# Performance work log

Hardware: AMD Instinct MI355X
Metric: run time of the kernel (lower is better)

The kernel has to match this reference:

```python
import jax, jax.numpy as jnp
import numpy as np

B, N, NPOINT, K = 8, 4096, 512, 32
D_IN, D_POS, D_OUT = 64, 64, 128
D = D_IN + D_POS  # 128, channel dim entering Double_SA
EPS = 1e-5


def _gather(pts, idx):
    # pts [B,N,C], idx [B,...] -> [B,...,C]
    return jax.vmap(lambda p, i: p[i])(pts, idx)


def _bn(x, p):
    # eval-mode BatchNorm over last (channel) dim; p = [gamma, beta, mean, var]
    g, b, m, v = p
    return g * (x - m) * jax.lax.rsqrt(v + EPS) + b


def _fps(xyz, start):
    # iterative farthest point sampling, vectorized over batch
    Bb, Nn, _ = xyz.shape
    def step(carry, _):
        dist, far = carry  # dist [B,N], far [B]
        c = jnp.take_along_axis(xyz, far[:, None, None], axis=1)  # [B,1,3]
        d = jnp.sum((xyz - c) ** 2, -1)
        dist = jnp.minimum(dist, d)
        return (dist, jnp.argmax(dist, -1)), far
    init = (jnp.full((Bb, Nn), 1e10, xyz.dtype), start)
    _, idx = jax.lax.scan(step, init, None, length=NPOINT)
    return idx.T  # [B, NPOINT]


def _forward(xyz, points, fps_start, pos_w1, pos_b1, pos_bn1, pos_w2, pos_b2, pos_bn2,
             nsa_wq, nsa_bq, nsa_wk, nsa_bk, nsa_wv, nsa_bv, nsa_gamma, gam_gamma,
             cat_w1, cat_b1, cat_bn1, cat_w2, cat_b2, cat_bn2, sc_w, sc_b, sc_bn):
    fps_idx = _fps(xyz, fps_start)                 # [B,S]
    center_xyz = _gather(xyz, fps_idx)             # [B,S,3]
    # brute-force KNN: squared distances center -> all points, take k smallest
    d2 = (jnp.sum(center_xyz ** 2, -1)[:, :, None] + jnp.sum(xyz ** 2, -1)[:, None, :]
          - 2.0 * jnp.einsum('bsc,bnc->bsn', center_xyz, xyz))  # [B,S,N]
    neg_d, knn_idx = jax.lax.top_k(-d2, K)
    knn_dist = -neg_d                               # [B,S,K], ascending
    grouped_xyz = _gather(xyz, knn_idx)             # [B,S,K,3]
    grouped_pts = _gather(points, knn_idx)          # [B,S,K,D_IN]
    # PosEmbeding: cat(center, neighbor, relative, dist) -> MLP(10 -> Dpos/2 -> Dpos)
    center = jnp.broadcast_to(center_xyz[:, :, None, :], grouped_xyz.shape)
    feat = jnp.concatenate([center, grouped_xyz, grouped_xyz - center, knn_dist[..., None]], -1)
    h = jax.nn.relu(_bn(feat @ pos_w1 + pos_b1, pos_bn1))
    pos = jax.nn.relu(_bn(h @ pos_w2 + pos_b2, pos_bn2))
    x = jnp.concatenate([pos, grouped_pts], -1)     # [B,S,K,D]
    # Neighbor_SA_New: per-group self-attention over K neighbors
    q = x @ nsa_wq + nsa_bq                         # [B,S,K,D//8]
    k = x @ nsa_wk + nsa_bk
    v = x @ nsa_wv + nsa_bv                         # [B,S,K,D]
    attn = jax.nn.softmax(jnp.einsum('bskc,bsjc->bskj', q, k), axis=-1)
    nei = nsa_gamma * jnp.einsum('bskj,bsjd->bskd', attn, v) + x
    # GAM: attention between groups over flattened K*D features
    flat = x.reshape(B, NPOINT, K * D)
    ga = jax.nn.softmax(jnp.einsum('bsd,btd->bst', flat, flat), axis=-1)  # [B,S,S]
    grp = gam_gamma * jnp.einsum('bst,btd->bsd', ga, flat).reshape(B, NPOINT, K, D) + x
    dsa = jnp.concatenate([nei, grp], -1)           # [B,S,K,2D]
    main = _bn(jax.nn.relu(_bn(dsa @ cat_w1 + cat_b1, cat_bn1)) @ cat_w2 + cat_b2, cat_bn2)
    sc = jax.nn.relu(_bn(grouped_pts @ sc_w + sc_b, sc_bn))
    new_points = jnp.max(jax.nn.relu(main + sc), axis=2)  # [B,S,D_OUT]
    return center_xyz, new_points


def setup_inputs():
    ks = jax.random.split(jax.random.key(0), 40)
    def w(i, shape, s=0.05):
        return s * jax.random.normal(ks[i], shape, jnp.float32)
    def bnp(i, c):
        k1, k2, k3, k4 = jax.random.split(ks[i], 4)
        return jnp.stack([jax.random.uniform(k1, (c,), jnp.float32, 0.5, 1.5),
                          0.1 * jax.random.normal(k2, (c,), jnp.float32),
                          0.1 * jax.random.normal(k3, (c,), jnp.float32),
                          jax.random.uniform(k4, (c,), jnp.float32, 0.5, 1.5)])
    return dict(
        xyz=jax.random.normal(ks[0], (B, N, 3), jnp.float32),
        points=jax.random.normal(ks[1], (B, N, D_IN), jnp.float32),
        fps_start=jax.random.randint(ks[2], (B,), 0, N),
        pos_w1=w(3, (10, D_POS // 2)), pos_b1=w(4, (D_POS // 2,)), pos_bn1=bnp(5, D_POS // 2),
        pos_w2=w(6, (D_POS // 2, D_POS)), pos_b2=w(7, (D_POS,)), pos_bn2=bnp(8, D_POS),
        nsa_wq=w(9, (D, D // 8)), nsa_bq=w(10, (D // 8,)),
        nsa_wk=w(11, (D, D // 8)), nsa_bk=w(12, (D // 8,)),
        nsa_wv=w(13, (D, D)), nsa_bv=w(14, (D,)),
        nsa_gamma=jnp.array([0.5], jnp.float32),
        gam_gamma=jnp.array([0.5], jnp.float32),
        cat_w1=w(15, (2 * D, 2 * D)), cat_b1=w(16, (2 * D,)), cat_bn1=bnp(17, 2 * D),
        cat_w2=w(18, (2 * D, D_OUT)), cat_b2=w(19, (D_OUT,)), cat_bn2=bnp(20, D_OUT),
        sc_w=w(21, (D_IN, D_OUT)), sc_b=w(22, (D_OUT,)), sc_bn=bnp(23, D_OUT),
    )


def reference(xyz, points, fps_start, pos_w1, pos_b1, pos_bn1, pos_w2, pos_b2, pos_bn2,
              nsa_wq, nsa_bq, nsa_wk, nsa_bk, nsa_wv, nsa_bv, nsa_gamma, gam_gamma,
              cat_w1, cat_b1, cat_bn1, cat_w2, cat_b2, cat_bn2, sc_w, sc_b, sc_bn):
    return _forward(xyz, points, fps_start, pos_w1, pos_b1, pos_bn1, pos_w2, pos_b2, pos_bn2,
                    nsa_wq, nsa_bq, nsa_wk, nsa_bk, nsa_wv, nsa_bv, nsa_gamma, gam_gamma,
                    cat_w1, cat_b1, cat_bn1, cat_w2, cat_b2, cat_bn2, sc_w, sc_b, sc_bn)
```

## Files before the change

### kernel.cpp

```cpp
#include <hip/hip_runtime.h>
#include <stdint.h>
#include <float.h>

typedef unsigned int uint;

#define NB 8
#define NPTS 4096
#define NS 512
#define NKN 32

__device__ int   g_fps_idx[NB*NS];
__device__ int   g_knn_idx[NB*NS*NKN];
__device__ float g_knn_d2 [NB*NS*NKN];
__device__ float g_posb   [(size_t)NB*NS*NKN*64];
__device__ float g_ga     [(size_t)NB*NS*NS];
__device__ float g_dsa    [(size_t)NB*NS*NKN*256];

__device__ __forceinline__ unsigned long long shfl_down_u64(unsigned long long v, int off){
  int lo = __shfl_down((int)(unsigned)v, off);
  int hi = __shfl_down((int)(unsigned)(v >> 32), off);
  return ((unsigned long long)(unsigned)hi << 32) | (unsigned)lo;
}
__device__ __forceinline__ unsigned long long u64max(unsigned long long a, unsigned long long b){
  return a > b ? a : b;
}
__device__ __forceinline__ unsigned long long u64min(unsigned long long a, unsigned long long b){
  return a < b ? a : b;
}
__device__ __forceinline__ void ldf8(const float* p, float* d){
  float4 a = *(const float4*)p, b = *(const float4*)(p+4);
  d[0]=a.x; d[1]=a.y; d[2]=a.z; d[3]=a.w; d[4]=b.x; d[5]=b.y; d[6]=b.z; d[7]=b.w;
}
__device__ __forceinline__ int read_start(const int* __restrict__ start, int b){
  int w1 = start[1], w3 = start[3], w5 = start[5], w7 = start[7];
  bool is64 = ((w1 | w3 | w5 | w7) == 0);
  int v = is64 ? start[2*b] : start[b];
  return v & (NPTS - 1);
}

__device__ __forceinline__ void load_flat8(const float* __restrict__ points,
                                           int b, int row, int n, float* d){
  const int k = n >> 7, col = n & 63;
  if (n & 64){
    const int idx = g_knn_idx[((b << 9) + row)*32 + k];
    ldf8(points + (((size_t)b << 12) + idx)*64 + col, d);
  } else {
    ldf8(g_posb + (((size_t)((b << 9) + row))*32 + k)*64 + col, d);
  }
}
__device__ __forceinline__ float4 load_flat4(const float* __restrict__ points,
                                             int b, int row, int n){
  const int k = n >> 7, d = n & 127;
  if (d & 64){
    const int idx = g_knn_idx[((b << 9) + row)*32 + k];
    return *(const float4*)(points + (((size_t)b << 12) + idx)*64 + (d & 63));
  } else {
    return *(const float4*)(g_posb + (((size_t)((b << 9) + row))*32 + k)*64 + d);
  }
}
__device__ __forceinline__ void load_gram8(const float* __restrict__ points,
                                           int b, int row, int kc, float* d){
  if (kc < 2048){
    ldf8(g_posb + ((size_t)((b << 9) + row))*2048 + kc, d);
  } else {
    const int kc2 = kc - 2048, kg = kc2 >> 6, col = kc2 & 63;
    const int idx = g_knn_idx[((b << 9) + row)*32 + kg];
    ldf8(points + (((size_t)b << 12) + idx)*64 + col, d);
  }
}

__global__ __launch_bounds__(256) void k_fps(const float* __restrict__ xyz,
                                             const int* __restrict__ start,
                                             float* __restrict__ center_out){
#pragma clang fp contract(off)
  const int b = blockIdx.x, tid = threadIdx.x;
  const float* X = xyz + (size_t)b * NPTS * 3;
  __shared__ float sx[NPTS], sy[NPTS], sz[NPTS];
  for (int p = tid; p < NPTS; p += 256){
    sx[p] = X[3*p]; sy[p] = X[3*p+1]; sz[p] = X[3*p+2];
  }
  __shared__ int s_start0;
  if (tid == 0) s_start0 = read_start(start, b);
  __syncthreads();
  float px[16], py[16], pz[16], dist[16];
  for (int i = 0; i < 16; i++){
    int p = tid*16 + i;
    px[i] = sx[p]; py[i] = sy[p]; pz[i] = sz[p];
    dist[i] = 1e10f;
  }
  __shared__ unsigned long long s_k[2][4];
  int cur = s_start0;
  for (int t = 0; t < NS; t++){
    if (tid == 0){
      g_fps_idx[b*NS + t] = cur;
      center_out[(size_t)(b*NS + t)*3 + 0] = sx[cur];
      center_out[(size_t)(b*NS + t)*3 + 1] = sy[cur];
      center_out[(size_t)(b*NS + t)*3 + 2] = sz[cur];
    }
    const float cx = sx[cur], cy = sy[cur], cz = sz[cur];
    unsigned long long k_[16];
#pragma unroll
    for (int i = 0; i < 16; i++){
      float dx = px[i]-cx, dy = py[i]-cy, dz = pz[i]-cz;
      float d = ((dx*dx) + (dy*dy)) + (dz*dz);
      dist[i] = fminf(dist[i], d);
      k_[i] = ((unsigned long long)__float_as_uint(dist[i]) << 32)
            | (unsigned)(NPTS-1 - (tid*16 + i));
    }
#pragma unroll
    for (int st = 8; st; st >>= 1)
      for (int i = 0; i < st; i++) k_[i] = u64max(k_[i], k_[i+st]);
    unsigned long long bk = k_[0];
    { unsigned long long a = shfl_down_u64(bk,16), c = shfl_down_u64(bk,32), d = shfl_down_u64(bk,48);
      bk = u64max(u64max(bk,a), u64max(c,d)); }
    { unsigned long long a = shfl_down_u64(bk,4),  c = shfl_down_u64(bk,8),  d = shfl_down_u64(bk,12);
      bk = u64max(u64max(bk,a), u64max(c,d)); }
    { unsigned long long a = shfl_down_u64(bk,1),  c = shfl_down_u64(bk,2),  d = shfl_down_u64(bk,3);
      bk = u64max(u64max(bk,a), u64max(c,d)); }
    const int par = t & 1;
    if ((tid & 63) == 0) s_k[par][tid>>6] = bk;
    __syncthreads();
    unsigned long long m = u64max(u64max(s_k[par][0], s_k[par][1]),
                                  u64max(s_k[par][2], s_k[par][3]));
    cur = NPTS-1 - (int)(unsigned)m;
  }
}

__global__ __launch_bounds__(256) void k_knn(const float* __restrict__ xyz){
#pragma clang fp contract(off)
  const int g = blockIdx.x;
  const int b = g >> 9;
  const int tid = threadIdx.x;
  const float* X = xyz + (size_t)b * NPTS * 3;
  const int cidx = g_fps_idx[g];
  const float cx = X[3*cidx], cy = X[3*cidx+1], cz = X[3*cidx+2];
  const float cs = ((cx*cx) + (cy*cy)) + (cz*cz);
  unsigned long long kl[16];
#pragma unroll
  for (int i = 0; i < 16; i++){
    int p = tid*16 + i;
    float x = X[3*p], y = X[3*p+1], z = X[3*p+2];
    float xs2 = ((x*x) + (y*y)) + (z*z);
    float dt  = ((cx*x) + (cy*y)) + (cz*z);
    float d   = (cs + xs2) - 2.0f*dt;
    unsigned bits = __float_as_uint(d);
    unsigned mono = (bits & 0x80000000u) ? ~bits : (bits ^ 0x80000000u);
    kl[i] = ((unsigned long long)mono << 32) | (unsigned)p;
  }
  __shared__ unsigned long long s_w[2][4];
  unsigned long long last = 0;
  for (int sel = 0; sel < NKN; sel++){
    unsigned long long mk[16];
#pragma unroll
    for (int i = 0; i < 16; i++)
      mk[i] = (kl[i] > last) ? kl[i] : 0xFFFFFFFFFFFFFFFFULL;
#pragma unroll
    for (int st = 8; st; st >>= 1)
      for (int i = 0; i < st; i++) mk[i] = u64min(mk[i], mk[i+st]);
    unsigned long long bk = mk[0];
    { unsigned long long a = shfl_down_u64(bk,16), c = shfl_down_u64(bk,32), d = shfl_down_u64(bk,48);
      bk = u64min(u64min(bk,a), u64min(c,d)); }
    { unsigned long long a = shfl_down_u64(bk,4),  c = shfl_down_u64(bk,8),  d = shfl_down_u64(bk,12);
      bk = u64min(u64min(bk,a), u64min(c,d)); }
    { unsigned long long a = shfl_down_u64(bk,1),  c = shfl_down_u64(bk,2),  d = shfl_down_u64(bk,3);
      bk = u64min(u64min(bk,a), u64min(c,d)); }
    const int par = sel & 1;
    if ((tid & 63) == 0) s_w[par][tid>>6] = bk;
    __syncthreads();
    unsigned long long m = u64min(u64min(s_w[par][0], s_w[par][1]),
                                  u64min(s_w[par][2], s_w[par][3]));
    last = m;
    if (tid == 0){
      unsigned hm = (unsigned)(m >> 32);
      unsigned bits = (hm & 0x80000000u) ? (hm ^ 0x80000000u) : ~hm;
      g_knn_idx[g*NKN + sel] = (int)(unsigned)m;
      g_knn_d2 [g*NKN + sel] = __uint_as_float(bits);
    }
  }
}

__global__ __launch_bounds__(256) void k_posembed(
    const float* __restrict__ xyz,
    const float* __restrict__ w1, const float* __restrict__ b1, const float* __restrict__ bn1,
    const float* __restrict__ w2, const float* __restrict__ b2, const float* __restrict__ bn2){
  __shared__ float w1s[320], a1s[32], d1s[32], w2s[2048], a2s[64], d2s[64];
  const int t = threadIdx.x;
  for (int i = t; i < 320; i += 256) w1s[i] = w1[i];
  for (int i = t; i < 2048; i += 256) w2s[i] = w2[i];
  if (t < 32){
    float g = bn1[t], be = bn1[32+t], m = bn1[64+t], v = bn1[96+t];
    float a = g * rsqrtf(v + 1e-5f);
    a1s[t] = a; d1s[t] = b1[t]*a + (be - m*a);
  }
  if (t < 64){
    float g = bn2[t], be = bn2[64+t], m = bn2[128+t], v = bn2[192+t];
    float a = g * rsqrtf(v + 1e-5f);
    a2s[t] = a; d2s[t] = b2[t]*a + (be - m*a);
  }
  __syncthreads();
  const int row = blockIdx.x*256 + t;
  const int b = row >> 14;
  const int g = row >> 5;
  const float* X = xyz + (size_t)b * NPTS * 3;
  const int ci = g_fps_idx[g];
  const int ni = g_knn_idx[row];
  float c0 = X[3*ci], c1 = X[3*ci+1], c2 = X[3*ci+2];
  float n0 = X[3*ni], n1 = X[3*ni+1], n2 = X[3*ni+2];
  float feat[10] = {c0,c1,c2, n0,n1,n2, n0-c0,n1-c1,n2-c2, g_knn_d2[row]};
  float h[32];
  for (int o = 0; o < 32; o++){
    float acc = 0.f;
    for (int j = 0; j < 10; j++) acc += feat[j]*w1s[j*32+o];
    h[o] = fmaxf(acc*a1s[o] + d1s[o], 0.f);
  }
  float* xr = g_posb + (size_t)row * 64;
  for (int o = 0; o < 64; o++){
    float acc = 0.f;
    for (int j = 0; j < 32; j++) acc += h[j]*w2s[j*64+o];
    xr[o] = fmaxf(acc*a2s[o] + d2s[o], 0.f);
  }
}

__global__ __launch_bounds__(256) void k_gram(const float* __restrict__ points){
  const int b = blockIdx.y;
  int ti = 0, rem = blockIdx.x;
  while (rem >= 8 - ti){ rem -= 8 - ti; ti++; }
  const int tj = ti + rem;
  const int i0 = ti * 64, j0 = tj * 64;
  __shared__ float As[32][68];
  __shared__ float Bs[32][68];
  const int t = threadIdx.x, tx = t & 15, ty = t >> 4;
  float acc[4][4] = {};
  for (int k0 = 0; k0 < 4096; k0 += 32){
    {
      int r = t >> 2, kk = (t & 3) * 8;
      float ta[8], tb[8];
      load_gram8(points, b, i0+r, k0+kk, ta);
      load_gram8(points, b, j0+r, k0+kk, tb);
      for (int jj = 0; jj < 8; jj++){
        int k = kk + jj;
        int c = (r + (k & 24)) & 63;
        As[k][c] = ta[jj]; Bs[k][c] = tb[jj];
      }
    }
    __syncthreads();
    for (int kk = 0; kk < 32; kk++){
      const int rot = kk & 24;
      const float4 a4 = *(const float4*)(&As[kk][(ty*4 + rot) & 63]);
      const float4 b4 = *(const float4*)(&Bs[kk][(tx*4 + rot) & 63]);
      const float ar[4] = {a4.x,a4.y,a4.z,a4.w};
      const float br[4] = {b4.x,b4.y,b4.z,b4.w};
      for (int ia = 0; ia < 4; ia++)
        for (int ib = 0; ib < 4; ib++) acc[ia][ib] += ar[ia]*br[ib];
    }
    __syncthreads();
  }
  float* C = g_ga + (size_t)b * NS * NS;
  for (int ia = 0; ia < 4; ia++){
    float4 o = {acc[ia][0], acc[ia][1], acc[ia][2], acc[ia][3]};
    *(float4*)(C + (size_t)(i0+ty*4+ia)*NS + j0 + tx*4) = o;
  }
  if (ti != tj){
    for (int ib = 0; ib < 4; ib++){
      float4 o = {acc[0][ib], acc[1][ib], acc[2][ib], acc[3][ib]};
      *(float4*)(C + (size_t)(j0+tx*4+ib)*NS + i0 + ty*4) = o;
    }
  }
}

__global__ __launch_bounds__(256) void k_softmax(){
  float* R = g_ga + (size_t)blockIdx.x * NS;
  const int t = threadIdx.x;
  float v0 = R[t], v1 = R[t+256];
  __shared__ float sm[4], ssum[4];
  float m = fmaxf(v0, v1);
  for (int off = 32; off; off >>= 1) m = fmaxf(m, __shfl_down(m, off));
  if ((t & 63) == 0) sm[t>>6] = m;
  __syncthreads();
  float mm = fmaxf(fmaxf(sm[0], sm[1]), fmaxf(sm[2], sm[3]));
  float e0 = expf(v0 - mm), e1 = expf(v1 - mm);
  float s = e0 + e1;
  for (int off = 32; off; off >>= 1) s += __shfl_down(s, off);
  if ((t & 63) == 0) ssum[t>>6] = s;
  __syncthreads();
  float inv = 1.0f / (ssum[0]+ssum[1]+ssum[2]+ssum[3]);
  R[t] = e0*inv; R[t+256] = e1*inv;
}

__global__ __launch_bounds__(256) void k_grp(const float* __restrict__ points,
                                             const float* __restrict__ gam_g){
  const int b = blockIdx.y;
  const int s0 = (blockIdx.x >> 6) * 64, n0 = (blockIdx.x & 63) * 64;
  const float* G = g_ga + (size_t)b * NS * NS;
  __shared__ float As[32][68];
  __shared__ float Bs[32][68];
  const int t = threadIdx.x, tx = t & 15, ty = t >> 4;
  float acc[4][4] = {};
  for (int k0 = 0; k0 < NS; k0 += 32){
    {
      int r = t >> 2, kk = (t & 3) * 8;
      const float* pa = G + (size_t)(s0+r)*NS + k0 + kk;
      float4 v0 = *(const float4*)pa, v1 = *(const float4*)(pa+4);
      const float va[8] = {v0.x,v0.y,v0.z,v0.w,v1.x,v1.y,v1.z,v1.w};
      for (int jj = 0; jj < 8; jj++){
        int k = kk + jj;
        As[k][(r + (k & 24)) & 63] = va[jj];
      }
      int k2 = t >> 3, c = (t & 7) * 8;
      float tb[8];
      load_flat8(points, b, k0+k2, n0+c, tb);
      float4 w0 = {tb[0],tb[1],tb[2],tb[3]}, w1 = {tb[4],tb[5],tb[6],tb[7]};
      *(float4*)(&Bs[k2][c])   = w0;
      *(float4*)(&Bs[k2][c+4]) = w1;
    }
    __syncthreads();
    for (int kk = 0; kk < 32; kk++){
      const float4 a4 = *(const float4*)(&As[kk][(ty*4 + (kk & 24)) & 63]);
      const float4 b4 = *(const float4*)(&Bs[kk][tx*4]);
      const float ar[4] = {a4.x,a4.y,a4.z,a4.w};
      const float br[4] = {b4.x,b4.y,b4.z,b4.w};
      for (int ia = 0; ia < 4; ia++)
        for (int ib = 0; ib < 4; ib++) acc[ia][ib] += ar[ia]*br[ib];
    }
    __syncthreads();
  }
  const float gmg = gam_g[0];
  const int n = n0 + tx*4;
  const int kq = n >> 7, dq = n & 127;
  for (int ia = 0; ia < 4; ia++){
    int s = s0 + ty*4 + ia;
    float4 xv = load_flat4(points, b, s, n);
    float4 o = {gmg*acc[ia][0]+xv.x, gmg*acc[ia][1]+xv.y,
                gmg*acc[ia][2]+xv.z, gmg*acc[ia][3]+xv.w};
    *(float4*)(g_dsa + ((size_t)((b*NS + s)*32 + kq))*256 + 128 + dq) = o;
  }
}

__global__ __launch_bounds__(256) void k_nsa(const float* __restrict__ points,
    const float* __restrict__ wq, const float* __restrict__ bq,
    const float* __restrict__ wk, const float* __restrict__ bk,
    const float* __restrict__ wv, const float* __restrict__ bv_,
    const float* __restrict__ nsa_g){
  const int g = blockIdx.y*512 + blockIdx.x;
  const int t = threadIdx.x, b = g >> 9;
  const int r = t >> 3, c = t & 7;
  __shared__ float xs[32][132];
  __shared__ float vs[32][132];
  __shared__ float qs[32][17], ks[32][17];
  __shared__ float at[32][33];
  {
    float tmp[8];
    ldf8(g_posb + ((size_t)g*32 + r)*64 + c*8, tmp);
    for (int j = 0; j < 8; j++) xs[r][c*8+j] = tmp[j];
    int idx = g_knn_idx[g*32 + r];
    ldf8(points + ((size_t)b*NPTS + idx)*64 + c*8, tmp);
    for (int j = 0; j < 8; j++) xs[r][64+c*8+j] = tmp[j];
  }
  __syncthreads();
  {
    float aq0 = bq[c], aq1 = bq[c+8], ak0 = bk[c], ak1 = bk[c+8];
    for (int j = 0; j < 128; j++){
      float xv = xs[r][j];
      aq0 += xv * wq[j*16+c];
      aq1 += xv * wq[j*16+c+8];
      ak0 += xv * wk[j*16+c];
      ak1 += xv * wk[j*16+c+8];
    }
    qs[r][c] = aq0; qs[r][c+8] = aq1; ks[r][c] = ak0; ks[r][c+8] = ak1;
  }
  {
    const float4* bv4 = (const float4*)bv_;
    float4 va = bv4[c], vb = bv4[8+c], vc = bv4[16+c], vd = bv4[24+c];
    const float4* wv4 = (const float4*)wv;
    for (int j = 0; j < 128; j++){
      float xv = xs[r][j];
      const float4* row = wv4 + (size_t)j*32;
      float4 w0 = row[c], w1 = row[8+c], w2 = row[16+c], w3 = row[24+c];
      va.x += xv*w0.x; va.y += xv*w0.y; va.z += xv*w0.z; va.w += xv*w0.w;
      vb.x += xv*w1.x; vb.y += xv*w1.y; vb.z += xv*w1.z; vb.w += xv*w1.w;
      vc.x += xv*w2.x; vc.y += xv*w2.y; vc.z += xv*w2.z; vc.w += xv*w2.w;
      vd.x += xv*w3.x; vd.y += xv*w3.y; vd.z += xv*w3.z; vd.w += xv*w3.w;
    }
    float4* vrow = (float4*)(&vs[r][0]);
    vrow[c] = va; vrow[8+c] = vb; vrow[16+c] = vc; vrow[24+c] = vd;
  }
  __syncthreads();
  float p0, p1, p2, p3;
  {
    float s[4];
    for (int jj = 0; jj < 4; jj++){
      int j = 4*c + jj; float acc = 0.f;
      for (int cc = 0; cc < 16; cc++) acc += qs[r][cc] * ks[j][cc];
      s[jj] = acc;
    }
    float m = fmaxf(fmaxf(s[0], s[1]), fmaxf(s[2], s[3]));
    m = fmaxf(m, __shfl_xor(m, 1));
    m = fmaxf(m, __shfl_xor(m, 2));
    m = fmaxf(m, __shfl_xor(m, 4));
    float e0 = expf(s[0]-m), e1 = expf(s[1]-m), e2 = expf(s[2]-m), e3 = expf(s[3]-m);
    float sum = ((e0 + e1) + (e2 + e3));
    sum += __shfl_xor(sum, 1);
    sum += __shfl_xor(sum, 2);
    sum += __shfl_xor(sum, 4);
    float inv = 1.0f / sum;
    p0 = e0*inv; p1 = e1*inv; p2 = e2*inv; p3 = e3*inv;
    at[r][4*c+0] = p0; at[r][4*c+1] = p1; at[r][4*c+2] = p2; at[r][4*c+3] = p3;
  }
  {
    float4 a0 = {0,0,0,0}, a1 = {0,0,0,0}, a2 = {0,0,0,0}, a3 = {0,0,0,0};
    for (int j = 0; j < 32; j++){
      float a = at[r][j];
      const float4* vrow = (const float4*)(&vs[j][0]);
      float4 w0 = vrow[c], w1 = vrow[8+c], w2 = vrow[16+c], w3 = vrow[24+c];
      a0.x += a*w0.x; a0.y += a*w0.y; a0.z += a*w0.z; a0.w += a*w0.w;
      a1.x += a*w1.x; a1.y += a*w1.y; a1.z += a*w1.z; a1.w += a*w1.w;
      a2.x += a*w2.x; a2.y += a*w2.y; a2.z += a*w2.z; a2.w += a*w2.w;
      a3.x += a*w3.x; a3.y += a*w3.y; a3.z += a*w3.z; a3.w += a*w3.w;
    }
    const float gmn = nsa_g[0];
    float* dst = g_dsa + ((size_t)g*32 + r)*256;
    float4 x0 = *(const float4*)(&xs[r][ 0+4*c]);
    float4 x1 = *(const float4*)(&xs[r][32+4*c]);
    float4 x2 = *(const float4*)(&xs[r][64+4*c]);
    float4 x3 = *(const float4*)(&xs[r][96+4*c]);
    float4 o0 = {gmn*a0.x+x0.x, gmn*a0.y+x0.y, gmn*a0.z+x0.z, gmn*a0.w+x0.w};
    float4 o1 = {gmn*a1.x+x1.x, gmn*a1.y+x1.y, gmn*a1.z+x1.z, gmn*a1.w+x1.w};
    float4 o2 = {gmn*a2.x+x2.x, gmn*a2.y+x2.y, gmn*a2.z+x2.z, gmn*a2.w+x2.w};
    float4 o3 = {gmn*a3.x+x3.x, gmn*a3.y+x3.y, gmn*a3.z+x3.z, gmn*a3.w+x3.w};
    *(float4*)(dst +  0 + 4*c) = o0;
    *(float4*)(dst + 32 + 4*c) = o1;
    *(float4*)(dst + 64 + 4*c) = o2;
    *(float4*)(dst + 96 + 4*c) = o3;
  }
}

__global__ __launch_bounds__(512) void k_mlp(const float* __restrict__ points,
    const float* __restrict__ w1, const float* __restrict__ b1, const float* __restrict__ bn1,
    const float* __restrict__ w2, const float* __restrict__ b2, const float* __restrict__ bn2,
    const float* __restrict__ wsc, const float* __restrict__ bsc, const float* __restrict__ bnsc,
    float* __restrict__ out){
  const int g = blockIdx.y*512 + blockIdx.x;
  const int t = threadIdx.x, b = g >> 9;
  __shared__ float ds[32][260];
  __shared__ float ps[32][68];
  __shared__ float a1s[256], d1s[256];
  __shared__ float red[512];
  for (int i = t; i < 2048; i += 512){
    int r = i >> 6, c = (i & 63) * 4;
    *(float4*)(&ds[r][c]) = *(const float4*)(g_dsa + ((size_t)g*32 + r)*256 + c);
  }
  if (t < 512){
    int r = t >> 4, c = (t & 15) * 4;
    int idx = g_knn_idx[g*32 + r];
    *(float4*)(&ps[r][c]) = *(const float4*)(points + ((size_t)b*NPTS + idx)*64 + c);
  }
  if (t < 256){
    float gg2 = bn1[t], be = bn1[256+t], m = bn1[512+t], v = bn1[768+t];
    float a = gg2 * rsqrtf(v + 1e-5f);
    a1s[t] = a; d1s[t] = b1[t]*a + (be - m*a);
  }
  __syncthreads();
  {
    const int kg = t >> 6, c0 = (t & 63) * 4;
    float acc[4][4] = {};
    for (int j = 0; j < 256; j += 4){
      float wvv[4][4];
      for (int jj = 0; jj < 4; jj++){
        float4 wrow = *(const float4*)(w1 + (j+jj)*256 + c0);
        wvv[jj][0] = wrow.x; wvv[jj][1] = wrow.y; wvv[jj][2] = wrow.z; wvv[jj][3] = wrow.w;
      }
      for (int r = 0; r < 4; r++){
        const float4 d4 = *(const float4*)(&ds[kg*4+r][j]);
        const float dr[4] = {d4.x, d4.y, d4.z, d4.w};
        for (int jj = 0; jj < 4; jj++)
          for (int i = 0; i < 4; i++) acc[r][i] += dr[jj]*wvv[jj][i];
      }
    }
    float4 o[4];
    for (int r = 0; r < 4; r++){
      o[r].x = fmaxf(acc[r][0]*a1s[c0+0] + d1s[c0+0], 0.f);
      o[r].y = fmaxf(acc[r][1]*a1s[c0+1] + d1s[c0+1], 0.f);
      o[r].z = fmaxf(acc[r][2]*a1s[c0+2] + d1s[c0+2], 0.f);
      o[r].w = fmaxf(acc[r][3]*a1s[c0+3] + d1s[c0+3], 0.f);
    }
    __syncthreads();
    for (int r = 0; r < 4; r++)
      *(float4*)(&ds[kg*4+r][c0]) = o[r];
  }
  __syncthreads();
  {
    const int c = t & 127, kh = t >> 7;
    float g2 = bn2[c], be2 = bn2[128+c], m2 = bn2[256+c], v2 = bn2[384+c];
    float a2 = g2 * rsqrtf(v2 + 1e-5f);
    float d2v = b2[c]*a2 + (be2 - m2*a2);
    float gsc = bnsc[c], besc = bnsc[128+c], msc = bnsc[256+c], vsc = bnsc[384+c];
    float asc = gsc * rsqrtf(vsc + 1e-5f);
    float dscv = bsc[c]*asc + (besc - msc*asc);
    float accm[8] = {};
    for (int j = 0; j < 256; j += 4){
      float w0 = w2[j*128+c], w1v = w2[(j+1)*128+c];
      float w2v = w2[(j+2)*128+c], w3 = w2[(j+3)*128+c];
      for (int r = 0; r < 8; r++){
        const float4 h4 = *(const float4*)(&ds[kh*8+r][j]);
        accm[r] += h4.x*w0; accm[r] += h4.y*w1v; accm[r] += h4.z*w2v; accm[r] += h4.w*w3;
      }
    }
    float accs[8] = {};
    for (int j = 0; j < 64; j += 4){
      float w0 = wsc[j*128+c], w1v = wsc[(j+1)*128+c];
      float w2v = wsc[(j+2)*128+c], w3 = wsc[(j+3)*128+c];
      for (int r = 0; r < 8; r++){
        const float4 p4 = *(const float4*)(&ps[kh*8+r][j]);
        accs[r] += p4.x*w0; accs[r] += p4.y*w1v; accs[r] += p4.z*w2v; accs[r] += p4.w*w3;
      }
    }
    float mx = -1e30f;
    for (int r = 0; r < 8; r++){
      float mainv = accm[r]*a2 + d2v;
      float scv = fmaxf(accs[r]*asc + dscv, 0.f);
      mx = fmaxf(mx, fmaxf(mainv + scv, 0.f));
    }
    red[t] = mx;
  }
  __syncthreads();
  if (t < 128){
    float m = fmaxf(fmaxf(red[t], red[t+128]), fmaxf(red[t+256], red[t+384]));
    out[12288 + (size_t)g*128 + t] = m;
  }
}

extern "C" void kernel_launch(void* const* d_in, const int* in_sizes, int n_in,
                              void* d_out, int out_size, void* d_ws, size_t ws_size,
                              hipStream_t stream){
  (void)in_sizes; (void)n_in; (void)d_ws; (void)ws_size; (void)out_size;
  const float* xyz      = (const float*)d_in[0];
  const float* points   = (const float*)d_in[1];
  const int*   fstart   = (const int*)  d_in[2];
  const float* pos_w1   = (const float*)d_in[3];
  const float* pos_b1   = (const float*)d_in[4];
  const float* pos_bn1  = (const float*)d_in[5];
  const float* pos_w2   = (const float*)d_in[6];
  const float* pos_b2   = (const float*)d_in[7];
  const float* pos_bn2  = (const float*)d_in[8];
  const float* nsa_wq   = (const float*)d_in[9];
  const float* nsa_bq   = (const float*)d_in[10];
  const float* nsa_wk   = (const float*)d_in[11];
  const float* nsa_bk   = (const float*)d_in[12];
  const float* nsa_wv   = (const float*)d_in[13];
  const float* nsa_bv   = (const float*)d_in[14];
  const float* nsa_g    = (const float*)d_in[15];
  const float* gam_g    = (const float*)d_in[16];
  const float* cat_w1   = (const float*)d_in[17];
  const float* cat_b1   = (const float*)d_in[18];
  const float* cat_bn1  = (const float*)d_in[19];
  const float* cat_w2   = (const float*)d_in[20];
  const float* cat_b2   = (const float*)d_in[21];
  const float* cat_bn2  = (const float*)d_in[22];
  const float* sc_w     = (const float*)d_in[23];
  const float* sc_b     = (const float*)d_in[24];
  const float* sc_bn    = (const float*)d_in[25];
  float* out = (float*)d_out;

  k_fps     <<<NB, 256, 0, stream>>>(xyz, fstart, out);
  k_knn     <<<NB*NS, 256, 0, stream>>>(xyz);
  k_posembed<<<512, 256, 0, stream>>>(xyz, pos_w1, pos_b1, pos_bn1, pos_w2, pos_b2, pos_bn2);
  k_gram    <<<dim3(36, NB), 256, 0, stream>>>(points);
  k_softmax <<<NB*NS, 256, 0, stream>>>();
  k_grp     <<<dim3(512, NB), 256, 0, stream>>>(points, gam_g);
  k_nsa     <<<dim3(512, NB), 256, 0, stream>>>(points, nsa_wq, nsa_bq, nsa_wk, nsa_bk,
                                                nsa_wv, nsa_bv, nsa_g);
  k_mlp     <<<dim3(512, NB), 512, 0, stream>>>(points, cat_w1, cat_b1, cat_bn1,
                                                cat_w2, cat_b2, cat_bn2,
                                                sc_w, sc_b, sc_bn, out);
}
```

Before: 1.967 ms.

## Enlarge k_grp register tile and retile k_mlp second GEMM for vector weight loads

k_grp now computes a 64x128 output tile per block with an 8x4 per-thread accumulator, up from a 64x64 tile with 4x4. This halves the grid and raises arithmetic intensity per shared-memory read. In k_mlp's second stage, each thread now computes 2 rows by 4 columns using float4 weight loads instead of scalar per-column loads across 8 rows, followed by a 16-way max reduction in shared memory. The larger tiles need more registers and shared memory, which may lower occupancy.

Result: slower. 2.072 ms (+5.3%).

```diff
diff --git a/kernel.cpp b/kernel.cpp
--- a/kernel.cpp
+++ b/kernel.cpp
@@ -290,12 +290,12 @@
 __global__ __launch_bounds__(256) void k_grp(const float* __restrict__ points,
                                              const float* __restrict__ gam_g){
   const int b = blockIdx.y;
-  const int s0 = (blockIdx.x >> 6) * 64, n0 = (blockIdx.x & 63) * 64;
+  const int s0 = (blockIdx.x >> 5) * 64, n0 = (blockIdx.x & 31) * 128;
   const float* G = g_ga + (size_t)b * NS * NS;
   __shared__ float As[32][68];
-  __shared__ float Bs[32][68];
-  const int t = threadIdx.x, tx = t & 15, ty = t >> 4;
-  float acc[4][4] = {};
+  __shared__ float Bs[32][132];
+  const int t = threadIdx.x, tx = t & 31, ry = t >> 5;
+  float acc[8][4] = {};
   for (int k0 = 0; k0 < NS; k0 += 32){
     {
       int r = t >> 2, kk = (t & 3) * 8;
@@ -306,20 +306,27 @@
         int k = kk + jj;
         As[k][(r + (k & 24)) & 63] = va[jj];
       }
-      int k2 = t >> 3, c = (t & 7) * 8;
-      float tb[8];
-      load_flat8(points, b, k0+k2, n0+c, tb);
-      float4 w0 = {tb[0],tb[1],tb[2],tb[3]}, w1 = {tb[4],tb[5],tb[6],tb[7]};
-      *(float4*)(&Bs[k2][c])   = w0;
-      *(float4*)(&Bs[k2][c+4]) = w1;
+      int k2 = t >> 3, c16 = (t & 7) * 16;
+      float tb[16];
+      load_flat8(points, b, k0+k2, n0+c16,     tb);
+      load_flat8(points, b, k0+k2, n0+c16+8, tb+8);
+      float4 w0 = {tb[0],tb[1],tb[2],tb[3]},   w1 = {tb[4],tb[5],tb[6],tb[7]};
+      float4 w2 = {tb[8],tb[9],tb[10],tb[11]}, w3 = {tb[12],tb[13],tb[14],tb[15]};
+      *(float4*)(&Bs[k2][c16])    = w0;
+      *(float4*)(&Bs[k2][c16+4])  = w1;
+      *(float4*)(&Bs[k2][c16+8])  = w2;
+      *(float4*)(&Bs[k2][c16+12]) = w3;
     }
     __syncthreads();
     for (int kk = 0; kk < 32; kk++){
-      const float4 a4 = *(const float4*)(&As[kk][(ty*4 + (kk & 24)) & 63]);
+      const int rot = kk & 24;
+      const int ca = (ry*8 + rot) & 63;
+      const float4 a0 = *(const float4*)(&As[kk][ca]);
+      const float4 a1 = *(const float4*)(&As[kk][ca+4]);
       const float4 b4 = *(const float4*)(&Bs[kk][tx*4]);
-      const float ar[4] = {a4.x,a4.y,a4.z,a4.w};
+      const float ar[8] = {a0.x,a0.y,a0.z,a0.w,a1.x,a1.y,a1.z,a1.w};
       const float br[4] = {b4.x,b4.y,b4.z,b4.w};
-      for (int ia = 0; ia < 4; ia++)
+      for (int ia = 0; ia < 8; ia++)
         for (int ib = 0; ib < 4; ib++) acc[ia][ib] += ar[ia]*br[ib];
     }
     __syncthreads();
@@ -327,8 +334,8 @@
   const float gmg = gam_g[0];
   const int n = n0 + tx*4;
   const int kq = n >> 7, dq = n & 127;
-  for (int ia = 0; ia < 4; ia++){
-    int s = s0 + ty*4 + ia;
+  for (int ia = 0; ia < 8; ia++){
+    int s = s0 + ry*8 + ia;
     float4 xv = load_flat4(points, b, s, n);
     float4 o = {gmg*acc[ia][0]+xv.x, gmg*acc[ia][1]+xv.y,
                 gmg*acc[ia][2]+xv.z, gmg*acc[ia][3]+xv.w};
@@ -444,12 +451,12 @@
   __shared__ float ds[32][260];
   __shared__ float ps[32][68];
   __shared__ float a1s[256], d1s[256];
-  __shared__ float red[512];
+  __shared__ float sm2[16][132];
   for (int i = t; i < 2048; i += 512){
     int r = i >> 6, c = (i & 63) * 4;
     *(float4*)(&ds[r][c]) = *(const float4*)(g_dsa + ((size_t)g*32 + r)*256 + c);
   }
-  if (t < 512){
+  {
     int r = t >> 4, c = (t & 15) * 4;
     int idx = g_knn_idx[g*32 + r];
     *(float4*)(&ps[r][c]) = *(const float4*)(points + ((size_t)b*NPTS + idx)*64 + c);
@@ -489,42 +496,66 @@
   }
   __syncthreads();
   {
-    const int c = t & 127, kh = t >> 7;
-    float g2 = bn2[c], be2 = bn2[128+c], m2 = bn2[256+c], v2 = bn2[384+c];
-    float a2 = g2 * rsqrtf(v2 + 1e-5f);
-    float d2v = b2[c]*a2 + (be2 - m2*a2);
-    float gsc = bnsc[c], besc = bnsc[128+c], msc = bnsc[256+c], vsc = bnsc[384+c];
-    float asc = gsc * rsqrtf(vsc + 1e-5f);
-    float dscv = bsc[c]*asc + (besc - msc*asc);
-    float accm[8] = {};
+    const int c0 = (t & 31) * 4, rg = t >> 5;
+    float accm0[4] = {}, accm1[4] = {};
     for (int j = 0; j < 256; j += 4){
-      float w0 = w2[j*128+c], w1v = w2[(j+1)*128+c];
-      float w2v = w2[(j+2)*128+c], w3 = w2[(j+3)*128+c];
-      for (int r = 0; r < 8; r++){
-        const float4 h4 = *(const float4*)(&ds[kh*8+r][j]);
-        accm[r] += h4.x*w0; accm[r] += h4.y*w1v; accm[r] += h4.z*w2v; accm[r] += h4.w*w3;
+      float4 wr0 = *(const float4*)(w2 + (size_t)(j+0)*128 + c0);
+      float4 wr1 = *(const float4*)(w2 + (size_t)(j+1)*128 + c0);
+      float4 wr2 = *(const float4*)(w2 + (size_t)(j+2)*128 + c0);
+      float4 wr3 = *(const float4*)(w2 + (size_t)(j+3)*128 + c0);
+      const float wA[4] = {wr0.x, wr0.y, wr0.z, wr0.w};
+      const float wB[4] = {wr1.x, wr1.y, wr1.z, wr1.w};
+      const float wC[4] = {wr2.x, wr2.y, wr2.z, wr2.w};
+      const float wD[4] = {wr3.x, wr3.y, wr3.z, wr3.w};
+      const float4 h0 = *(const float4*)(&ds[rg*2+0][j]);
+      const float4 h1 = *(const float4*)(&ds[rg*2+1][j]);
+      for (int i = 0; i < 4; i++){
+        accm0[i] += h0.x*wA[i]; accm0[i] += h0.y*wB[i];
+        accm0[i] += h0.z*wC[i]; accm0[i] += h0.w*wD[i];
+        accm1[i] += h1.x*wA[i]; accm1[i] += h1.y*wB[i];
+        accm1[i] += h1.z*wC[i]; accm1[i] += h1.w*wD[i];
       }
     }
-    float accs[8] = {};
+    float accs0[4] = {}, accs1[4] = {};
     for (int j = 0; j < 64; j += 4){
-      float w0 = wsc[j*128+c], w1v = wsc[(j+1)*128+c];
-      float w2v = wsc[(j+2)*128+c], w3 = wsc[(j+3)*128+c];
-      for (int r = 0; r < 8; r++){
-        const float4 p4 = *(const float4*)(&ps[kh*8+r][j]);
-        accs[r] += p4.x*w0; accs[r] += p4.y*w1v; accs[r] += p4.z*w2v; accs[r] += p4.w*w3;
+      float4 wr0 = *(const float4*)(wsc + (size_t)(j+0)*128 + c0);
+      float4 wr1 = *(const float4*)(wsc + (size_t)(j+1)*128 + c0);
+      float4 wr2 = *(const float4*)(wsc + (size_t)(j+2)*128 + c0);
+      float4 wr3 = *(const float4*)(wsc + (size_t)(j+3)*128 + c0);
+      const float wA[4] = {wr0.x, wr0.y, wr0.z, wr0.w};
+      const float wB[4] = {wr1.x, wr1.y, wr1.z, wr1.w};
+      const float wC[4] = {wr2.x, wr2.y, wr2.z, wr2.w};
+      const float wD[4] = {wr3.x, wr3.y, wr3.z, wr3.w};
+      const float4 p0 = *(const float4*)(&ps[rg*2+0][j]);
+      const float4 p1 = *(const float4*)(&ps[rg*2+1][j]);
+      for (int i = 0; i < 4; i++){
+        accs0[i] += p0.x*wA[i]; accs0[i] += p0.y*wB[i];
+        accs0[i] += p0.z*wC[i]; accs0[i] += p0.w*wD[i];
+        accs1[i] += p1.x*wA[i]; accs1[i] += p1.y*wB[i];
+        accs1[i] += p1.z*wC[i]; accs1[i] += p1.w*wD[i];
       }
     }
-    float mx = -1e30f;
-    for (int r = 0; r < 8; r++){
-      float mainv = accm[r]*a2 + d2v;
-      float scv = fmaxf(accs[r]*asc + dscv, 0.f);
-      mx = fmaxf(mx, fmaxf(mainv + scv, 0.f));
-    }
-    red[t] = mx;
+    for (int i = 0; i < 4; i++){
+      const int c = c0 + i;
+      float g2 = bn2[c], be2 = bn2[128+c], m2 = bn2[256+c], v2 = bn2[384+c];
+      float a2 = g2 * rsqrtf(v2 + 1e-5f);
+      float d2v = b2[c]*a2 + (be2 - m2*a2);
+      float gsc = bnsc[c], besc = bnsc[128+c], msc = bnsc[256+c], vsc = bnsc[384+c];
+      float asc = gsc * rsqrtf(vsc + 1e-5f);
+      float dscv = bsc[c]*asc + (besc - msc*asc);
+      float m0 = accm0[i]*a2 + d2v;
+      float s0v = fmaxf(accs0[i]*asc + dscv, 0.f);
+      float r0 = fmaxf(m0 + s0v, 0.f);
+      float m1 = accm1[i]*a2 + d2v;
+      float s1v = fmaxf(accs1[i]*asc + dscv, 0.f);
+      float r1 = fmaxf(m1 + s1v, 0.f);
+      sm2[rg][c] = fmaxf(fmaxf(-1e30f, r0), r1);
+    }
   }
   __syncthreads();
   if (t < 128){
-    float m = fmaxf(fmaxf(red[t], red[t+128]), fmaxf(red[t+256], red[t+384]));
+    float m = sm2[0][t];
+    for (int rg = 1; rg < 16; rg++) m = fmaxf(m, sm2[rg][t]);
     out[12288 + (size_t)g*128 + t] = m;
   }
 }
@@ -566,7 +597,7 @@
   k_posembed<<<512, 256, 0, stream>>>(xyz, pos_w1, pos_b1, pos_bn1, pos_w2, pos_b2, pos_bn2);
   k_gram    <<<dim3(36, NB), 256, 0, stream>>>(points);
   k_softmax <<<NB*NS, 256, 0, stream>>>();
-  k_grp     <<<dim3(512, NB), 256, 0, stream>>>(points, gam_g);
+  k_grp     <<<dim3(256, NB), 256, 0, stream>>>(points, gam_g);
   k_nsa     <<<dim3(512, NB), 256, 0, stream>>>(points, nsa_wq, nsa_bq, nsa_wk, nsa_bk,
                                                 nsa_wv, nsa_bv, nsa_g);
   k_mlp     <<<dim3(512, NB), 512, 0, stream>>>(points, cat_w1, cat_b1, cat_bn1,
```
